# Performance work log

Hardware: AMD Instinct MI355X
Metric: run time of the kernel (lower is better)

The kernel has to match this reference:

```python
import jax, jax.numpy as jnp
import numpy as np

N, D, H, E, K = 16384, 1024, 4096, 8, 2
EPS = 1e-5


def setup_inputs() -> dict:
    key = jax.random.key(0)
    ks = jax.random.split(key, 12)
    s = 0.02
    return {
        "x": jax.random.normal(ks[0], (N, D), dtype=jnp.float32),
        "ln_g": jnp.ones((D,), jnp.float32),
        "ln_b": jnp.zeros((D,), jnp.float32),
        "r_w1": jax.random.normal(ks[1], (D, H // 2), jnp.float32) * s,
        "r_b1": jnp.zeros((H // 2,), jnp.float32),
        "r_w2": jax.random.normal(ks[2], (H // 2, E), jnp.float32) * s,
        "r_b2": jnp.zeros((E,), jnp.float32),
        "e_w1": jax.random.normal(ks[3], (E, D, H), jnp.float32) * s,
        "e_b1": jnp.zeros((E, H), jnp.float32),
        "e_w2": jax.random.normal(ks[4], (E, H, D), jnp.float32) * s,
        "e_b2": jnp.zeros((E, D), jnp.float32),
    }


def reference(x, ln_g, ln_b, r_w1, r_b1, r_w2, r_b2, e_w1, e_b1, e_w2, e_b2):
    # LayerNorm
    mu = jnp.mean(x, axis=-1, keepdims=True)
    var = jnp.mean(jnp.square(x - mu), axis=-1, keepdims=True)
    xn = (x - mu) * jax.lax.rsqrt(var + EPS) * ln_g + ln_b  # [N, D]

    # Router: Linear -> ReLU -> Linear -> softmax -> top-k, renormalize
    logits = jax.nn.relu(xn @ r_w1 + r_b1) @ r_w2 + r_b2  # [N, E]
    probs = jax.nn.softmax(logits, axis=-1)
    vals, idx = jax.lax.top_k(probs, K)  # [N, K]
    vals = vals / jnp.sum(vals, axis=-1, keepdims=True)

    # Dense expert dispatch: loop over fixed small E, weight by combine gate
    out = jnp.zeros_like(x)
    for e in range(E):
        gate = jnp.sum(vals * (idx == e).astype(vals.dtype), axis=-1)  # [N]
        h = jax.nn.relu(xn @ e_w1[e] + e_b1[e])  # dropout in eval mode -> identity
        y = h @ e_w2[e] + e_b2[e]  # [N, D]
        out = out + gate[:, None] * y
    return x + out
```

## Files before the change

### kernel.cpp

```cpp
#include <hip/hip_runtime.h>
#include <cstdint>
#include <cstddef>

typedef unsigned short u16;
typedef __attribute__((ext_vector_type(8))) short bf16x8;
typedef __attribute__((ext_vector_type(4))) float f32x4;

#define N_TOK 16384
#define DIM   1024
#define HID   4096
#define NEXP  8
#define HR    2048
#define TAU   0.02f
#define MAXMT 264

__device__ __forceinline__ u16 f2bf(float f) {
  union { float f; uint32_t u; } x; x.f = f;
  uint32_t r = x.u + 0x7FFFu + ((x.u >> 16) & 1u);
  return (u16)(r >> 16);
}
__device__ __forceinline__ float bf2f(u16 u) {
  union { uint32_t u; float f; } x; x.u = ((uint32_t)u) << 16; return x.f;
}

__device__ __forceinline__ void async16(const void* g, const void* l) {
  auto gp = reinterpret_cast<const __attribute__((address_space(1))) uint32_t*>(
      reinterpret_cast<uintptr_t>(g));
  auto lp = reinterpret_cast<__attribute__((address_space(3))) uint32_t*>(
      reinterpret_cast<uintptr_t>(l));
  __builtin_amdgcn_global_load_lds(gp, lp, 16, 0, 0);
}

__device__ __forceinline__ unsigned xcd_swz(unsigned flat, unsigned nwg) {
  const unsigned xcd = flat & 7u, lid = flat >> 3;
  const unsigned q = nwg >> 3, r = nwg & 7u;
  return (xcd < r ? xcd * (q + 1u) : r * (q + 1u) + (xcd - r) * q) + lid;
}

template<bool SPLIT>
__global__ __launch_bounds__(256)
void transpose_cvt(const float* __restrict__ src, u16* __restrict__ hi,
                   u16* __restrict__ lo, int R, int C)
{
  __shared__ float tile[32][33];
  const size_t bofs = (size_t)blockIdx.z * R * C;
  src += bofs; hi += bofs; if (SPLIT) lo += bofs;
  const int tx = threadIdx.x, ty = threadIdx.y;
  const int c0 = blockIdx.x * 32, r0 = blockIdx.y * 32;
#pragma unroll
  for (int i = 0; i < 4; ++i)
    tile[ty + i * 8][tx] = src[(size_t)(r0 + ty + i * 8) * C + c0 + tx];
  __syncthreads();
#pragma unroll
  for (int i = 0; i < 4; ++i) {
    float v = tile[tx][ty + i * 8];
    size_t o = (size_t)(c0 + ty + i * 8) * R + r0 + tx;
    u16 h = f2bf(v);
    hi[o] = h;
    if (SPLIT) lo[o] = f2bf(v - bf2f(h));
  }
}

__global__ __launch_bounds__(256)
void ln_kernel(const float* __restrict__ x, const float* __restrict__ g,
               const float* __restrict__ b, u16* __restrict__ xh,
               u16* __restrict__ xl, float* __restrict__ out)
{
  const int row = blockIdx.x;
  const int t = threadIdx.x;
  const float4 xv = ((const float4*)(x + (size_t)row * DIM))[t];
  float s = xv.x + xv.y + xv.z + xv.w;
  float q = xv.x * xv.x + xv.y * xv.y + xv.z * xv.z + xv.w * xv.w;
#pragma unroll
  for (int off = 32; off; off >>= 1) {
    s += __shfl_down(s, off, 64);
    q += __shfl_down(q, off, 64);
  }
  __shared__ float sm[8];
  __shared__ float mu_s, rs_s;
  const int lane = t & 63, wv = t >> 6;
  if (lane == 0) { sm[wv] = s; sm[wv + 4] = q; }
  __syncthreads();
  if (t == 0) {
    float S = sm[0] + sm[1] + sm[2] + sm[3];
    float Q = sm[4] + sm[5] + sm[6] + sm[7];
    float mu = S * (1.f / DIM);
    float var = Q * (1.f / DIM) - mu * mu;
    mu_s = mu; rs_s = rsqrtf(var + 1e-5f);
  }
  __syncthreads();
  const float mu = mu_s, rs = rs_s;
  const float4 gv = ((const float4*)g)[t];
  const float4 bv = ((const float4*)b)[t];
  float n0 = (xv.x - mu) * rs * gv.x + bv.x;
  float n1 = (xv.y - mu) * rs * gv.y + bv.y;
  float n2 = (xv.z - mu) * rs * gv.z + bv.z;
  float n3 = (xv.w - mu) * rs * gv.w + bv.w;
  ushort4 h, l;
  h.x = f2bf(n0); l.x = f2bf(n0 - bf2f(h.x));
  h.y = f2bf(n1); l.y = f2bf(n1 - bf2f(h.y));
  h.z = f2bf(n2); l.z = f2bf(n2 - bf2f(h.z));
  h.w = f2bf(n3); l.w = f2bf(n3 - bf2f(h.w));
  ((ushort4*)(xh + (size_t)row * DIM))[t] = h;
  ((ushort4*)(xl + (size_t)row * DIM))[t] = l;
  ((float4*)(out + (size_t)row * DIM))[t] = xv;
}

__global__ __launch_bounds__(256)
void logits_kernel(const u16* __restrict__ HrB, const float* __restrict__ w2,
                   float* __restrict__ logits)
{
  const int row = blockIdx.x, t = threadIdx.x;
  const u16* h = HrB + (size_t)row * HR;
  const ushort4* hv = (const ushort4*)(h + t * 8);
  ushort4 h0 = hv[0], h1 = hv[1];
  u16 hh[8] = {h0.x, h0.y, h0.z, h0.w, h1.x, h1.y, h1.z, h1.w};
  float p[8] = {0, 0, 0, 0, 0, 0, 0, 0};
#pragma unroll
  for (int j = 0; j < 8; ++j) {
    const int col = t * 8 + j;
    const float v = bf2f(hh[j]);
    const float4* wp = (const float4*)(w2 + (size_t)col * 8);
    float4 a = wp[0], b = wp[1];
    p[0] += v * a.x; p[1] += v * a.y; p[2] += v * a.z; p[3] += v * a.w;
    p[4] += v * b.x; p[5] += v * b.y; p[6] += v * b.z; p[7] += v * b.w;
  }
#pragma unroll
  for (int off = 32; off; off >>= 1)
#pragma unroll
    for (int e = 0; e < 8; ++e) p[e] += __shfl_down(p[e], off, 64);
  __shared__ float sm[4][8];
  const int lane = t & 63, wv = t >> 6;
  if (lane == 0) {
#pragma unroll
    for (int e = 0; e < 8; ++e) sm[wv][e] = p[e];
  }
  __syncthreads();
  if (t < 8)
    logits[(size_t)row * 8 + t] = sm[0][t] + sm[1][t] + sm[2][t] + sm[3][t];
}

__device__ __forceinline__ void load_logits(const float* logits, const float* b2,
                                            int row, float l[8]) {
  const float4* lp = (const float4*)(logits + (size_t)row * 8);
  float4 a = lp[0], b = lp[1];
  l[0] = a.x + b2[0]; l[1] = a.y + b2[1]; l[2] = a.z + b2[2]; l[3] = a.w + b2[3];
  l[4] = b.x + b2[4]; l[5] = b.y + b2[5]; l[6] = b.z + b2[6]; l[7] = b.w + b2[7];
}
__device__ __forceinline__ void top2(const float l[8], int& i0, float& l0,
                                     int& i1, float& l1) {
  i0 = 0; l0 = l[0];
#pragma unroll
  for (int e = 1; e < 8; ++e) if (l[e] > l0) { l0 = l[e]; i0 = e; }
  i1 = -1; l1 = -1e30f;
#pragma unroll
  for (int e = 0; e < 8; ++e) if (e != i0 && l[e] > l1) { l1 = l[e]; i1 = e; }
}

__global__ __launch_bounds__(256)
void pass_flag(float* __restrict__ logits, const float* __restrict__ b2,
               int* __restrict__ fixL, int* __restrict__ cntFix)
{
  __shared__ int lcnt;
  __shared__ int base;
  const int t = threadIdx.x;
  const int row = blockIdx.x * 256 + t;
  if (t == 0) lcnt = 0;
  float l[8]; load_logits(logits, b2, row, l);
  int i0, i1; float l0, l1;
  top2(l, i0, l0, i1, l1);
  float l2 = -1e30f;
#pragma unroll
  for (int e = 0; e < 8; ++e)
    if (e != i0 && e != i1 && l[e] > l2) l2 = l[e];
  const bool flag = (l1 - l2) < TAU;
  __syncthreads();
  int r = 0;
  if (flag) r = atomicAdd(&lcnt, 1);
  __syncthreads();
  if (t == 0) base = atomicAdd(cntFix, lcnt);
  __syncthreads();
  if (flag) {
    fixL[base + r] = row;
    float4 z = {0.f, 0.f, 0.f, 0.f};
    ((float4*)(logits + (size_t)row * 8))[0] = z;
    ((float4*)(logits + (size_t)row * 8))[1] = z;
  }
}

__global__ __launch_bounds__(256)
void pass_count(const float* __restrict__ logits, const float* __restrict__ b2,
                int* __restrict__ cnts)
{
  __shared__ int lcnt[NEXP];
  const int t = threadIdx.x;
  const int row = blockIdx.x * 256 + t;
  if (t < NEXP) lcnt[t] = 0;
  float l[8]; load_logits(logits, b2, row, l);
  int i0, i1; float l0, l1;
  top2(l, i0, l0, i1, l1);
  __syncthreads();
  atomicAdd(&lcnt[i0], 1);
  atomicAdd(&lcnt[i1], 1);
  __syncthreads();
  if (t < NEXP) atomicAdd(&cnts[t], lcnt[t]);
}

__global__ void scan_kernel(const int* __restrict__ cnts, int* __restrict__ offs,
                            int* __restrict__ tileOffs)
{
  if (threadIdx.x == 0) {
    int s = 0, ts = 0;
#pragma unroll
    for (int e = 0; e < NEXP; ++e) {
      offs[e] = s; s += cnts[e];
      tileOffs[e] = ts; ts += (cnts[e] + 127) >> 7;
    }
    offs[NEXP] = s;
    tileOffs[NEXP] = ts;
  }
}

__global__ __launch_bounds__(256)
void pass_scatter(const float* __restrict__ logits, const float* __restrict__ b2,
                  const int* __restrict__ offs, int* __restrict__ cnts2,
                  int* __restrict__ rowsC, float* __restrict__ gateC)
{
  __shared__ int lcnt[NEXP];
  __shared__ int sbase[NEXP];
  const int t = threadIdx.x;
  const int row = blockIdx.x * 256 + t;
  if (t < NEXP) lcnt[t] = 0;
  float l[8]; load_logits(logits, b2, row, l);
  int i0, i1; float l0, l1;
  top2(l, i0, l0, i1, l1);
  float tt = expf(l1 - l0);
  float g0 = 1.f / (1.f + tt);
  float g1 = tt / (1.f + tt);
  __syncthreads();
  int r0 = atomicAdd(&lcnt[i0], 1);
  int r1 = atomicAdd(&lcnt[i1], 1);
  __syncthreads();
  if (t < NEXP) sbase[t] = atomicAdd(&cnts2[t], lcnt[t]);
  __syncthreads();
  int p0 = offs[i0] + sbase[i0] + r0;
  int p1 = offs[i1] + sbase[i1] + r1;
  rowsC[p0] = row; gateC[p0] = g0;
  rowsC[p1] = row; gateC[p1] = g1;
}

template<int EPI, bool GATHER>
__global__ __launch_bounds__(512, 4)
void gemm_moe(const u16* __restrict__ A0, const u16* __restrict__ B0,
              int lda, int ldb, int K, int NT,
              size_t bStrideE, int biasStrideE,
              const int* __restrict__ counts,
              const int* __restrict__ offs, const int* __restrict__ tileOffs,
              const int* __restrict__ rowsC, const float* __restrict__ gatesC,
              const float* __restrict__ bias,
              u16* __restrict__ Cbf, float* __restrict__ Cf32, int ldc)
{
  const unsigned swz = xcd_swz(blockIdx.x, gridDim.x);
  const int mt = (int)(swz / (unsigned)NT);
  if (mt >= tileOffs[NEXP]) return;
  int e = 0;
#pragma unroll
  for (int i = 1; i < NEXP; ++i) if (tileOffs[i] <= mt) e = i;
  const int m0 = (mt - tileOffs[e]) * 128;
  const int n0 = (int)(swz % (unsigned)NT) * 256;
  const int Mq = counts[e];
  if (m0 >= Mq) return;

  const int off = offs[e];
  const int* rows = rowsC + off;
  const u16* B = B0 + (size_t)e * bStrideE;
  const float* bi = bias + (size_t)e * biasStrideE;

  __shared__ alignas(16) u16 As[4][128 * 32];
  __shared__ alignas(16) u16 Bs[3][256 * 32];

  const int t = threadIdx.x;
  const int numK = K >> 5;

  const int rloc = t >> 2;
  const int cb = ((t & 3) << 4) ^ (((t >> 5) & 1) << 5);
  const int csrc = cb >> 1;
  const int arow0 = m0 + rloc;
  const int amc = arow0 < Mq ? arow0 : (Mq - 1);
  const size_t agr = GATHER ? (size_t)rows[amc] : (size_t)(off + amc);
  const u16* aSrc = A0 + agr * lda + csrc;
  const u16* bSrc0 = B + (size_t)(n0 + rloc) * ldb + csrc;
  const u16* bSrc1 = B + (size_t)(n0 + 128 + rloc) * ldb + csrc;

  const int lane = t & 63, wv = t >> 6;
  const int wm = wv >> 2;
  const int wn = wv & 3;
  const int fr = lane & 15, fq = lane >> 4;

  int aIdx[4], bIdx[4];
#pragma unroll
  for (int mf = 0; mf < 4; ++mf) {
    const int r = wm * 64 + mf * 16 + fr;
    aIdx[mf] = r * 32 + ((fq * 8) ^ (((r >> 3) & 1) << 4));
  }
#pragma unroll
  for (int nf = 0; nf < 4; ++nf) {
    const int rb = wn * 64 + nf * 16 + fr;
    bIdx[nf] = rb * 32 + ((fq * 8) ^ (((rb >> 3) & 1) << 4));
  }

  f32x4 acc[4][4];
#pragma unroll
  for (int i = 0; i < 4; ++i)
#pragma unroll
    for (int j = 0; j < 4; ++j) acc[i][j] = (f32x4){0.f, 0.f, 0.f, 0.f};

#pragma unroll
  for (int h = 0; h < 3; ++h)
    async16(aSrc + h * 32, &As[h][t * 8]);
#pragma unroll
  for (int h = 0; h < 2; ++h) {
    async16(bSrc0 + h * 32, &Bs[h][t * 8]);
    async16(bSrc1 + h * 32, &Bs[h][4096 + t * 8]);
  }
  asm volatile("s_waitcnt vmcnt(2)" ::: "memory");
  __builtin_amdgcn_s_barrier();
  __builtin_amdgcn_sched_barrier(0);

  int bR = 0;
  int bW = 2;
  for (int T = 0; T < numK; ++T) {
    if (T + 2 < numK) {
      async16(bSrc0 + (T + 2) * 32, &Bs[bW][t * 8]);
      async16(bSrc1 + (T + 2) * 32, &Bs[bW][4096 + t * 8]);
    }
    if (T + 3 < numK) async16(aSrc + (T + 3) * 32, &As[(T + 3) & 3][t * 8]);

    const u16* aLds = As[T & 3];
    const u16* bLds = Bs[bR];
    bf16x8 aF[4], bF[4];
#pragma unroll
    for (int i = 0; i < 4; ++i) {
      aF[i] = *(const bf16x8*)&aLds[aIdx[i]];
      bF[i] = *(const bf16x8*)&bLds[bIdx[i]];
    }
    __builtin_amdgcn_s_setprio(1);
#pragma unroll
    for (int mf = 0; mf < 4; ++mf)
#pragma unroll
      for (int nf = 0; nf < 4; ++nf)
        acc[mf][nf] = __builtin_amdgcn_mfma_f32_16x16x32_bf16(
            aF[mf], bF[nf], acc[mf][nf], 0, 0, 0);
    __builtin_amdgcn_s_setprio(0);
    __builtin_amdgcn_sched_barrier(0);

    const int rem = numK - T;
    if (rem >= 4) {
      if (T == 0) { asm volatile("s_waitcnt vmcnt(3)" ::: "memory"); }
      else        { asm volatile("s_waitcnt vmcnt(4)" ::: "memory"); }
    }
    else if (rem == 3) { asm volatile("s_waitcnt vmcnt(3)" ::: "memory"); }
    else               { asm volatile("s_waitcnt vmcnt(0)" ::: "memory"); }
    __builtin_amdgcn_s_barrier();
    __builtin_amdgcn_sched_barrier(0);

    bR = (bR == 2) ? 0 : bR + 1;
    bW = (bW == 2) ? 0 : bW + 1;
  }

  float bv[4];
#pragma unroll
  for (int nf = 0; nf < 4; ++nf) bv[nf] = bi[n0 + wn * 64 + nf * 16 + fr];

#pragma unroll
  for (int mf = 0; mf < 4; ++mf)
#pragma unroll
    for (int r = 0; r < 4; ++r) {
      const int m = m0 + wm * 64 + mf * 16 + fq * 4 + r;
      if (m < Mq) {
        if constexpr (EPI == 2) {
          const size_t orow = (size_t)rows[m];
          const float g = gatesC[off + m];
#pragma unroll
          for (int nf = 0; nf < 4; ++nf) {
            const int n = n0 + wn * 64 + nf * 16 + fr;
            atomicAdd(&Cf32[orow * ldc + n], g * (acc[mf][nf][r] + bv[nf]));
          }
        } else {
#pragma unroll
          for (int nf = 0; nf < 4; ++nf) {
            const int n = n0 + wn * 64 + nf * 16 + fr;
            Cbf[(size_t)(off + m) * ldc + n] =
                f2bf(fmaxf(acc[mf][nf][r] + bv[nf], 0.f));
          }
        }
      }
    }
}

template<bool SPLIT, int EPI, bool GATHER>
__global__ __launch_bounds__(256, 2)
void gemm_bt(const u16* __restrict__ A0, const u16* __restrict__ A1,
             const u16* __restrict__ B0, const u16* __restrict__ B1,
             int lda, int ldb, int K, int M,
             const int* __restrict__ counts, int expertArg,
             const int* __restrict__ offs,
             const int* __restrict__ rowsC, const float* __restrict__ gatesC,
             const float* __restrict__ bias,
             const float* __restrict__ w2, float* __restrict__ logits,
             u16* __restrict__ Cbf, float* __restrict__ Cf32, int ldc)
{
  int expert, m0, n0;
  if (counts == nullptr) {
    const unsigned nwg = gridDim.x * gridDim.y;
    const unsigned flat = blockIdx.y * gridDim.x + blockIdx.x;
    const unsigned swz = xcd_swz(flat, nwg);
    expert = expertArg;
    m0 = (int)(swz / gridDim.x) * 128;
    n0 = (int)(swz % gridDim.x) * 128;
  } else {
    expert = expertArg;
    m0 = blockIdx.y * 128;
    n0 = blockIdx.x * 128;
  }

  const int Mq = counts ? counts[expert] : M;
  if (m0 >= Mq) return;
  const int off = offs ? offs[expert] : 0;
  const int* rows = rowsC ? rowsC + off : nullptr;
  const float* gates = gatesC ? gatesC + off : nullptr;
  const u16* B = B0;
  const u16* Bl = SPLIT ? B1 : nullptr;
  const float* bi = bias;
  const int z = (int)blockIdx.z;
  const int zOff = z * K;

  __shared__ u16 As0[128 * 32], Bs0[128 * 32];
  __shared__ u16 As1[SPLIT ? 128 * 32 : 8], Bs1[SPLIT ? 128 * 32 : 8];

  const int t = threadIdx.x;
  size_t aoff[2]; int acodd[2]; size_t boff[2];
#pragma unroll
  for (int i = 0; i < 2; ++i) {
    int gdx = i * 256 + t;
    int ar = gdx >> 2, ac = (gdx & 3) * 8;
    int am = m0 + ar;
    int amc = am < Mq ? am : (Mq - 1);
    int agr = GATHER ? rows[amc] : amc;
    aoff[i] = (size_t)agr * lda + ac + zOff;
    boff[i] = (size_t)(n0 + ar) * ldb + ac + zOff;
    acodd[i] = gdx * 8;
  }

  f32x4 acc[4][4];
#pragma unroll
  for (int i = 0; i < 4; ++i)
#pragma unroll
    for (int j = 0; j < 4; ++j) acc[i][j] = (f32x4){0.f, 0.f, 0.f, 0.f};

  const int lane = t & 63, wv = t >> 6;
  const int wm = (wv >> 1) * 64, wn = (wv & 1) * 64;
  const int fr = lane & 15, fq = lane >> 4;

  for (int k0 = 0; k0 < K; k0 += 32) {
    __syncthreads();
#pragma unroll
    for (int i = 0; i < 2; ++i) {
      async16(A0 + aoff[i] + k0, &As0[acodd[i]]);
      async16(B + boff[i] + k0, &Bs0[acodd[i]]);
      if (SPLIT) {
        async16(A1 + aoff[i] + k0, &As1[acodd[i]]);
        async16(Bl + boff[i] + k0, &Bs1[acodd[i]]);
      }
    }
    __syncthreads();
    bf16x8 af[4], bfr[4], af1[4], bf1[4];
#pragma unroll
    for (int xi = 0; xi < 4; ++xi) {
      af[xi]  = *(const bf16x8*)&As0[(wm + xi * 16 + fr) * 32 + fq * 8];
      bfr[xi] = *(const bf16x8*)&Bs0[(wn + xi * 16 + fr) * 32 + fq * 8];
      if (SPLIT) {
        af1[xi] = *(const bf16x8*)&As1[(wm + xi * 16 + fr) * 32 + fq * 8];
        bf1[xi] = *(const bf16x8*)&Bs1[(wn + xi * 16 + fr) * 32 + fq * 8];
      }
    }
#pragma unroll
    for (int mt = 0; mt < 4; ++mt)
#pragma unroll
      for (int nt = 0; nt < 4; ++nt) {
        acc[mt][nt] = __builtin_amdgcn_mfma_f32_16x16x32_bf16(af[mt], bfr[nt], acc[mt][nt], 0, 0, 0);
        if (SPLIT) {
          acc[mt][nt] = __builtin_amdgcn_mfma_f32_16x16x32_bf16(af[mt], bf1[nt], acc[mt][nt], 0, 0, 0);
          acc[mt][nt] = __builtin_amdgcn_mfma_f32_16x16x32_bf16(af1[mt], bfr[nt], acc[mt][nt], 0, 0, 0);
        }
      }
  }

  if constexpr (EPI == 3) {
    float w2v[4][8]; float b1v[4];
#pragma unroll
    for (int nt = 0; nt < 4; ++nt) {
      const int n = n0 + wn + nt * 16 + fr;
      b1v[nt] = bi[n];
      const float4* wp = (const float4*)(w2 + (size_t)n * 8);
      float4 wa = wp[0], wb = wp[1];
      w2v[nt][0] = wa.x; w2v[nt][1] = wa.y; w2v[nt][2] = wa.z; w2v[nt][3] = wa.w;
      w2v[nt][4] = wb.x; w2v[nt][5] = wb.y; w2v[nt][6] = wb.z; w2v[nt][7] = wb.w;
    }
#pragma unroll
    for (int mt = 0; mt < 4; ++mt) {
      float pe[4][8];
#pragma unroll
      for (int r = 0; r < 4; ++r)
#pragma unroll
        for (int ee = 0; ee < 8; ++ee) pe[r][ee] = 0.f;
#pragma unroll
      for (int nt = 0; nt < 4; ++nt)
#pragma unroll
        for (int r = 0; r < 4; ++r) {
          float v = fmaxf(acc[mt][nt][r] + b1v[nt], 0.f);
#pragma unroll
          for (int ee = 0; ee < 8; ++ee) pe[r][ee] += v * w2v[nt][ee];
        }
#pragma unroll
      for (int offx = 1; offx < 16; offx <<= 1)
#pragma unroll
        for (int r = 0; r < 4; ++r)
#pragma unroll
          for (int ee = 0; ee < 8; ++ee)
            pe[r][ee] += __shfl_xor(pe[r][ee], offx, 64);
      if (fr == 0) {
#pragma unroll
        for (int r = 0; r < 4; ++r) {
          const int m = m0 + wm + mt * 16 + fq * 4 + r;
          if (m < Mq) {
            const int lrow = GATHER ? rows[m] : m;
#pragma unroll
            for (int ee = 0; ee < 8; ++ee)
              atomicAdd(&logits[(size_t)lrow * 8 + ee], pe[r][ee]);
          }
        }
      }
    }
    return;
  }

#pragma unroll
  for (int mt = 0; mt < 4; ++mt) {
#pragma unroll
    for (int nt = 0; nt < 4; ++nt) {
      const int n = n0 + wn + nt * 16 + fr;
      const float bvv = (z == 0) ? bi[n] : 0.f;
#pragma unroll
      for (int r = 0; r < 4; ++r) {
        const int m = m0 + wm + mt * 16 + fq * 4 + r;
        if (m < Mq) {
          float v = acc[mt][nt][r] + bvv;
          if constexpr (EPI == 1) {
            Cbf[(size_t)m * ldc + n] = f2bf(fmaxf(v, 0.f));
          } else {
            atomicAdd(&Cf32[(size_t)rows[m] * ldc + n], gates[m] * v);
          }
        }
      }
    }
  }
}

extern "C" void kernel_launch(void* const* d_in, const int* in_sizes, int n_in,
                              void* d_out, int out_size, void* d_ws, size_t ws_size,
                              hipStream_t stream)
{
  const float* x    = (const float*)d_in[0];
  const float* ln_g = (const float*)d_in[1];
  const float* ln_b = (const float*)d_in[2];
  const float* r_w1 = (const float*)d_in[3];
  const float* r_b1 = (const float*)d_in[4];
  const float* r_w2 = (const float*)d_in[5];
  const float* r_b2 = (const float*)d_in[6];
  const float* e_w1 = (const float*)d_in[7];
  const float* e_b1 = (const float*)d_in[8];
  const float* e_w2 = (const float*)d_in[9];
  const float* e_b2 = (const float*)d_in[10];
  float* out = (float*)d_out;

  char* ws = (char*)d_ws;
  const size_t MB = 1024ull * 1024ull;
  u16*   xnhi = (u16*)(ws);
  u16*   xnlo = (u16*)(ws + 32 * MB);
  u16*   rw1h = (u16*)(ws + 64 * MB);
  u16*   rw1l = (u16*)(ws + 68 * MB);
  u16*   ew1t = (u16*)(ws + 72 * MB);
  u16*   ew2t = (u16*)(ws + 136 * MB);
  float* logits = (float*)(ws + 200 * MB);
  int*   rowsC  = (int*)(ws + 200 * MB + 512 * 1024);
  float* gateC  = (float*)(ws + 200 * MB + 640 * 1024);
  int*   fixL   = (int*)(ws + 200 * MB + 768 * 1024);
  int*   cntb   = (int*)(ws + 200 * MB + 832 * 1024);
  int*   cnts   = cntb;
  int*   cnts2  = cntb + 8;
  int*   offs   = cntb + 16;
  int*   cntFix = cntb + 25;
  int*   tileOffs = cntb + 32;
  u16*   Hbuf = (u16*)(ws + 201 * MB);
  u16*   HrB  = Hbuf;
  (void)in_sizes; (void)n_in; (void)out_size;

  const bool fused = ws_size >= 458ull * MB;

  hipMemsetAsync(cntb, 0, 256, stream);

  dim3 tb(32, 8);
  transpose_cvt<true ><<<dim3(HR / 32, DIM / 32, 1), tb, 0, stream>>>(r_w1, rw1h, rw1l, DIM, HR);
  transpose_cvt<false><<<dim3(HID / 32, DIM / 32, NEXP), tb, 0, stream>>>(e_w1, ew1t, nullptr, DIM, HID);
  transpose_cvt<false><<<dim3(DIM / 32, HID / 32, NEXP), tb, 0, stream>>>(e_w2, ew2t, nullptr, HID, DIM);

  ln_kernel<<<N_TOK, 256, 0, stream>>>(x, ln_g, ln_b, xnhi, xnlo, out);

  gemm_bt<false, 1, false><<<dim3(HR / 128, N_TOK / 128), 256, 0, stream>>>(
      xnhi, nullptr, rw1h, nullptr, DIM, DIM, DIM, N_TOK,
      nullptr, 0, nullptr, nullptr, nullptr, r_b1, nullptr, nullptr,
      HrB, nullptr, HR);

  logits_kernel<<<N_TOK, 256, 0, stream>>>(HrB, r_w2, logits);

  pass_flag<<<N_TOK / 256, 256, 0, stream>>>(logits, r_b2, fixL, cntFix);

  gemm_bt<true, 3, true><<<dim3(HR / 128, N_TOK / 128), 256, 0, stream>>>(
      xnhi, xnlo, rw1h, rw1l, DIM, DIM, DIM, N_TOK,
      cntFix, 0, nullptr, fixL, nullptr, r_b1, r_w2, logits,
      nullptr, nullptr, 0);

  pass_count<<<N_TOK / 256, 256, 0, stream>>>(logits, r_b2, cnts);
  scan_kernel<<<1, 64, 0, stream>>>(cnts, offs, tileOffs);
  pass_scatter<<<N_TOK / 256, 256, 0, stream>>>(logits, r_b2, offs, cnts2, rowsC, gateC);

  if (fused) {
    gemm_moe<1, true><<<dim3((HID / 256) * MAXMT), 512, 0, stream>>>(
        xnhi, ew1t, DIM, DIM, DIM, HID / 256,
        (size_t)HID * DIM, HID,
        cnts, offs, tileOffs, rowsC, nullptr, e_b1,
        Hbuf, nullptr, HID);
    gemm_moe<2, false><<<dim3((DIM / 256) * MAXMT), 512, 0, stream>>>(
        Hbuf, ew2t, HID, HID, HID, DIM / 256,
        (size_t)DIM * HID, DIM,
        cnts, offs, tileOffs, rowsC, gateC, e_b2,
        nullptr, out, DIM);
  } else {
    for (int e = 0; e < NEXP; ++e) {
      gemm_bt<false, 1, true><<<dim3(HID / 128, N_TOK / 128), 256, 0, stream>>>(
          xnhi, nullptr, ew1t + (size_t)e * HID * DIM, nullptr,
          DIM, DIM, DIM, N_TOK,
          cnts, e, offs, rowsC, nullptr, e_b1 + (size_t)e * HID, nullptr, nullptr,
          Hbuf, nullptr, HID);
      gemm_bt<false, 2, false><<<dim3(DIM / 128, N_TOK / 128, 2), 256, 0, stream>>>(
          Hbuf, nullptr, ew2t + (size_t)e * DIM * HID, nullptr,
          HID, HID, HID / 2, N_TOK,
          cnts, e, offs, rowsC, gateC, e_b2 + (size_t)e * DIM, nullptr, nullptr,
          nullptr, out, DIM);
    }
  }
}
```

Baseline: 1.371 ms.

## Halve MoE GEMM block to 4 waves with 128x64 per-wave tiles

The expert GEMM now runs with 256 threads (4 waves) instead of 512 (8 waves) per 128x256 tile. Each wave owns a 128x64 slice, so it holds 8x4 accumulator fragments and issues more MFMAs per LDS fragment load, raising register reuse. Each thread also issues twice as many async global-to-LDS copies, and the vmcnt waits are rescaled to match. The trade is fewer waves to hide latency and higher register pressure under launch_bounds(256,2).

```diff
diff --git a/kernel.cpp b/kernel.cpp
--- a/kernel.cpp
+++ b/kernel.cpp
@@ -250,7 +250,7 @@
 }
 
 template<int EPI, bool GATHER>
-__global__ __launch_bounds__(512, 4)
+__global__ __launch_bounds__(256, 2)
 void gemm_moe(const u16* __restrict__ A0, const u16* __restrict__ B0,
               int lda, int ldb, int K, int NT,
               size_t bStrideE, int biasStrideE,
@@ -282,25 +282,36 @@
   const int t = threadIdx.x;
   const int numK = K >> 5;
 
-  const int rloc = t >> 2;
-  const int cb = ((t & 3) << 4) ^ (((t >> 5) & 1) << 5);
-  const int csrc = cb >> 1;
-  const int arow0 = m0 + rloc;
-  const int amc = arow0 < Mq ? arow0 : (Mq - 1);
-  const size_t agr = GATHER ? (size_t)rows[amc] : (size_t)(off + amc);
-  const u16* aSrc = A0 + agr * lda + csrc;
-  const u16* bSrc0 = B + (size_t)(n0 + rloc) * ldb + csrc;
-  const u16* bSrc1 = B + (size_t)(n0 + 128 + rloc) * ldb + csrc;
+  const u16* aptr[2]; int adst[2];
+#pragma unroll
+  for (int i = 0; i < 2; ++i) {
+    const int gdx = i * 256 + t;
+    const int ar = gdx >> 2;
+    const int cb = ((gdx & 3) << 4) ^ (((gdx >> 5) & 1) << 5);
+    const int am = m0 + ar;
+    const int amc = am < Mq ? am : (Mq - 1);
+    const size_t agr = GATHER ? (size_t)rows[amc] : (size_t)(off + amc);
+    aptr[i] = A0 + agr * lda + (cb >> 1);
+    adst[i] = gdx * 8;
+  }
+  const u16* bptr[4]; int bdst[4];
+#pragma unroll
+  for (int i = 0; i < 4; ++i) {
+    const int gdx = i * 256 + t;
+    const int br = gdx >> 2;
+    const int cb = ((gdx & 3) << 4) ^ (((gdx >> 5) & 1) << 5);
+    bptr[i] = B + (size_t)(n0 + br) * ldb + (cb >> 1);
+    bdst[i] = gdx * 8;
+  }
 
   const int lane = t & 63, wv = t >> 6;
-  const int wm = wv >> 2;
-  const int wn = wv & 3;
+  const int wn = wv;
   const int fr = lane & 15, fq = lane >> 4;
 
-  int aIdx[4], bIdx[4];
-#pragma unroll
-  for (int mf = 0; mf < 4; ++mf) {
-    const int r = wm * 64 + mf * 16 + fr;
+  int aIdx[8], bIdx[4];
+#pragma unroll
+  for (int mf = 0; mf < 8; ++mf) {
+    const int r = mf * 16 + fr;
     aIdx[mf] = r * 32 + ((fq * 8) ^ (((r >> 3) & 1) << 4));
   }
 #pragma unroll
@@ -309,21 +320,23 @@
     bIdx[nf] = rb * 32 + ((fq * 8) ^ (((rb >> 3) & 1) << 4));
   }
 
-  f32x4 acc[4][4];
-#pragma unroll
-  for (int i = 0; i < 4; ++i)
+  f32x4 acc[8][4];
+#pragma unroll
+  for (int i = 0; i < 8; ++i)
 #pragma unroll
     for (int j = 0; j < 4; ++j) acc[i][j] = (f32x4){0.f, 0.f, 0.f, 0.f};
 
 #pragma unroll
-  for (int h = 0; h < 3; ++h)
-    async16(aSrc + h * 32, &As[h][t * 8]);
-#pragma unroll
-  for (int h = 0; h < 2; ++h) {
-    async16(bSrc0 + h * 32, &Bs[h][t * 8]);
-    async16(bSrc1 + h * 32, &Bs[h][4096 + t * 8]);
-  }
-  asm volatile("s_waitcnt vmcnt(2)" ::: "memory");
+  for (int h = 0; h < 3; ++h) {
+    async16(aptr[0] + h * 32, &As[h][adst[0]]);
+    async16(aptr[1] + h * 32, &As[h][adst[1]]);
+  }
+#pragma unroll
+  for (int h = 0; h < 2; ++h)
+#pragma unroll
+    for (int i = 0; i < 4; ++i)
+      async16(bptr[i] + h * 32, &Bs[h][bdst[i]]);
+  asm volatile("s_waitcnt vmcnt(4)" ::: "memory");
   __builtin_amdgcn_s_barrier();
   __builtin_amdgcn_sched_barrier(0);
 
@@ -331,22 +344,26 @@
   int bW = 2;
   for (int T = 0; T < numK; ++T) {
     if (T + 2 < numK) {
-      async16(bSrc0 + (T + 2) * 32, &Bs[bW][t * 8]);
-      async16(bSrc1 + (T + 2) * 32, &Bs[bW][4096 + t * 8]);
-    }
-    if (T + 3 < numK) async16(aSrc + (T + 3) * 32, &As[(T + 3) & 3][t * 8]);
-
-    const u16* aLds = As[T & 3];
-    const u16* bLds = Bs[bR];
-    bf16x8 aF[4], bF[4];
-#pragma unroll
-    for (int i = 0; i < 4; ++i) {
-      aF[i] = *(const bf16x8*)&aLds[aIdx[i]];
-      bF[i] = *(const bf16x8*)&bLds[bIdx[i]];
-    }
+#pragma unroll
+      for (int i = 0; i < 4; ++i)
+        async16(bptr[i] + (size_t)(T + 2) * 32, &Bs[bW][bdst[i]]);
+    }
+    if (T + 3 < numK) {
+      async16(aptr[0] + (size_t)(T + 3) * 32, &As[(T + 3) & 3][adst[0]]);
+      async16(aptr[1] + (size_t)(T + 3) * 32, &As[(T + 3) & 3][adst[1]]);
+    }
+
+    const u16* aL = As[T & 3];
+    const u16* bL = Bs[bR];
+    bf16x8 aF[8], bF[4];
+#pragma unroll
+    for (int mf = 0; mf < 8; ++mf) aF[mf] = *(const bf16x8*)&aL[aIdx[mf]];
+#pragma unroll
+    for (int nf = 0; nf < 4; ++nf) bF[nf] = *(const bf16x8*)&bL[bIdx[nf]];
+
     __builtin_amdgcn_s_setprio(1);
 #pragma unroll
-    for (int mf = 0; mf < 4; ++mf)
+    for (int mf = 0; mf < 8; ++mf)
 #pragma unroll
       for (int nf = 0; nf < 4; ++nf)
         acc[mf][nf] = __builtin_amdgcn_mfma_f32_16x16x32_bf16(
@@ -355,11 +372,9 @@
     __builtin_amdgcn_sched_barrier(0);
 
     const int rem = numK - T;
-    if (rem >= 4) {
-      if (T == 0) { asm volatile("s_waitcnt vmcnt(3)" ::: "memory"); }
-      else        { asm volatile("s_waitcnt vmcnt(4)" ::: "memory"); }
-    }
-    else if (rem == 3) { asm volatile("s_waitcnt vmcnt(3)" ::: "memory"); }
+    if (T == 0)        { asm volatile("s_waitcnt vmcnt(6)" ::: "memory"); }
+    else if (rem >= 4) { asm volatile("s_waitcnt vmcnt(8)" ::: "memory"); }
+    else if (rem == 3) { asm volatile("s_waitcnt vmcnt(6)" ::: "memory"); }
     else               { asm volatile("s_waitcnt vmcnt(0)" ::: "memory"); }
     __builtin_amdgcn_s_barrier();
     __builtin_amdgcn_sched_barrier(0);
@@ -373,10 +388,10 @@
   for (int nf = 0; nf < 4; ++nf) bv[nf] = bi[n0 + wn * 64 + nf * 16 + fr];
 
 #pragma unroll
-  for (int mf = 0; mf < 4; ++mf)
+  for (int mf = 0; mf < 8; ++mf)
 #pragma unroll
     for (int r = 0; r < 4; ++r) {
-      const int m = m0 + wm * 64 + mf * 16 + fq * 4 + r;
+      const int m = m0 + mf * 16 + fq * 4 + r;
       if (m < Mq) {
         if constexpr (EPI == 2) {
           const size_t orow = (size_t)rows[m];
@@ -636,12 +651,12 @@
   pass_scatter<<<N_TOK / 256, 256, 0, stream>>>(logits, r_b2, offs, cnts2, rowsC, gateC);
 
   if (fused) {
-    gemm_moe<1, true><<<dim3((HID / 256) * MAXMT), 512, 0, stream>>>(
+    gemm_moe<1, true><<<dim3((HID / 256) * MAXMT), 256, 0, stream>>>(
         xnhi, ew1t, DIM, DIM, DIM, HID / 256,
         (size_t)HID * DIM, HID,
         cnts, offs, tileOffs, rowsC, nullptr, e_b1,
         Hbuf, nullptr, HID);
-    gemm_moe<2, false><<<dim3((DIM / 256) * MAXMT), 512, 0, stream>>>(
+    gemm_moe<2, false><<<dim3((DIM / 256) * MAXMT), 256, 0, stream>>>(
         Hbuf, ew2t, HID, HID, HID, DIM / 256,
         (size_t)DIM * HID, DIM,
         cnts, offs, tileOffs, rowsC, gateC, e_b2,
```

After: 1.373 ms. Within noise of the previous version (+0.1%).

## Shrink MoE GEMM tiles to 128x128 with 256 threads and reuse for router GEMM

Applied to the files above, without the earlier changes.

Changes the grouped MoE GEMM from 128x256 tiles with 512 threads to 128x128 tiles with 256 threads. A and B now share a uniform 3-stage LDS pipeline, and the wait counts are rewritten to match. A DENSE template variant is added and replaces the older gemm_bt kernel for the router's first linear layer. Smaller tiles launch more blocks and use less LDS per block, which may raise occupancy. In exchange, each block reuses operands less and more global traffic goes to B.

```diff
diff --git a/kernel.cpp b/kernel.cpp
--- a/kernel.cpp
+++ b/kernel.cpp
@@ -249,10 +249,10 @@
   rowsC[p1] = row; gateC[p1] = g1;
 }
 
-template<int EPI, bool GATHER>
-__global__ __launch_bounds__(512, 4)
+template<int EPI, bool GATHER, bool DENSE>
+__global__ __launch_bounds__(256, 3)
 void gemm_moe(const u16* __restrict__ A0, const u16* __restrict__ B0,
-              int lda, int ldb, int K, int NT,
+              int lda, int ldb, int K, int NT, int Mdense,
               size_t bStrideE, int biasStrideE,
               const int* __restrict__ counts,
               const int* __restrict__ offs, const int* __restrict__ tileOffs,
@@ -262,39 +262,49 @@
 {
   const unsigned swz = xcd_swz(blockIdx.x, gridDim.x);
   const int mt = (int)(swz / (unsigned)NT);
-  if (mt >= tileOffs[NEXP]) return;
-  int e = 0;
-#pragma unroll
-  for (int i = 1; i < NEXP; ++i) if (tileOffs[i] <= mt) e = i;
-  const int m0 = (mt - tileOffs[e]) * 128;
-  const int n0 = (int)(swz % (unsigned)NT) * 256;
-  const int Mq = counts[e];
-  if (m0 >= Mq) return;
-
-  const int off = offs[e];
-  const int* rows = rowsC + off;
+  int e, m0, Mq, off;
+  if constexpr (DENSE) {
+    if (mt >= Mdense / 128) return;
+    e = 0; m0 = mt * 128; Mq = Mdense; off = 0;
+  } else {
+    if (mt >= tileOffs[NEXP]) return;
+    e = 0;
+#pragma unroll
+    for (int i = 1; i < NEXP; ++i) if (tileOffs[i] <= mt) e = i;
+    m0 = (mt - tileOffs[e]) * 128;
+    Mq = counts[e];
+    if (m0 >= Mq) return;
+    off = offs[e];
+  }
+  const int n0 = (int)(swz % (unsigned)NT) * 128;
+  const int* rows = DENSE ? nullptr : (rowsC + off);
   const u16* B = B0 + (size_t)e * bStrideE;
   const float* bi = bias + (size_t)e * biasStrideE;
 
-  __shared__ alignas(16) u16 As[4][128 * 32];
-  __shared__ alignas(16) u16 Bs[3][256 * 32];
+  __shared__ alignas(16) u16 As[3][128 * 32];
+  __shared__ alignas(16) u16 Bs[3][128 * 32];
 
   const int t = threadIdx.x;
   const int numK = K >> 5;
 
-  const int rloc = t >> 2;
-  const int cb = ((t & 3) << 4) ^ (((t >> 5) & 1) << 5);
-  const int csrc = cb >> 1;
-  const int arow0 = m0 + rloc;
-  const int amc = arow0 < Mq ? arow0 : (Mq - 1);
-  const size_t agr = GATHER ? (size_t)rows[amc] : (size_t)(off + amc);
-  const u16* aSrc = A0 + agr * lda + csrc;
-  const u16* bSrc0 = B + (size_t)(n0 + rloc) * ldb + csrc;
-  const u16* bSrc1 = B + (size_t)(n0 + 128 + rloc) * ldb + csrc;
+  const u16* aptr[2]; const u16* bptr[2]; int sdst[2];
+#pragma unroll
+  for (int i = 0; i < 2; ++i) {
+    const int gdx = i * 256 + t;
+    const int r = gdx >> 2;
+    const int cb = ((gdx & 3) << 4) ^ (((gdx >> 5) & 1) << 5);
+    const int cs = cb >> 1;
+    int amc = (m0 + r) < Mq ? (m0 + r) : (Mq - 1);
+    const size_t agr = DENSE ? (size_t)(m0 + r)
+                             : (GATHER ? (size_t)rows[amc] : (size_t)(off + amc));
+    aptr[i] = A0 + agr * lda + cs;
+    bptr[i] = B + (size_t)(n0 + r) * ldb + cs;
+    sdst[i] = gdx * 8;
+  }
 
   const int lane = t & 63, wv = t >> 6;
-  const int wm = wv >> 2;
-  const int wn = wv & 3;
+  const int wm = wv >> 1;
+  const int wn = wv & 1;
   const int fr = lane & 15, fq = lane >> 4;
 
   int aIdx[4], bIdx[4];
@@ -316,33 +326,33 @@
     for (int j = 0; j < 4; ++j) acc[i][j] = (f32x4){0.f, 0.f, 0.f, 0.f};
 
 #pragma unroll
-  for (int h = 0; h < 3; ++h)
-    async16(aSrc + h * 32, &As[h][t * 8]);
-#pragma unroll
   for (int h = 0; h < 2; ++h) {
-    async16(bSrc0 + h * 32, &Bs[h][t * 8]);
-    async16(bSrc1 + h * 32, &Bs[h][4096 + t * 8]);
-  }
-  asm volatile("s_waitcnt vmcnt(2)" ::: "memory");
+    async16(bptr[0] + h * 32, &Bs[h][sdst[0]]);
+    async16(bptr[1] + h * 32, &Bs[h][sdst[1]]);
+    async16(aptr[0] + h * 32, &As[h][sdst[0]]);
+    async16(aptr[1] + h * 32, &As[h][sdst[1]]);
+  }
+  asm volatile("s_waitcnt vmcnt(4)" ::: "memory");
   __builtin_amdgcn_s_barrier();
   __builtin_amdgcn_sched_barrier(0);
 
-  int bR = 0;
-  int bW = 2;
+  int sR = 0;
+  int sW = 2;
   for (int T = 0; T < numK; ++T) {
     if (T + 2 < numK) {
-      async16(bSrc0 + (T + 2) * 32, &Bs[bW][t * 8]);
-      async16(bSrc1 + (T + 2) * 32, &Bs[bW][4096 + t * 8]);
-    }
-    if (T + 3 < numK) async16(aSrc + (T + 3) * 32, &As[(T + 3) & 3][t * 8]);
-
-    const u16* aLds = As[T & 3];
-    const u16* bLds = Bs[bR];
+      async16(bptr[0] + (size_t)(T + 2) * 32, &Bs[sW][sdst[0]]);
+      async16(bptr[1] + (size_t)(T + 2) * 32, &Bs[sW][sdst[1]]);
+      async16(aptr[0] + (size_t)(T + 2) * 32, &As[sW][sdst[0]]);
+      async16(aptr[1] + (size_t)(T + 2) * 32, &As[sW][sdst[1]]);
+    }
+
+    const u16* aL = As[sR];
+    const u16* bL = Bs[sR];
     bf16x8 aF[4], bF[4];
 #pragma unroll
     for (int i = 0; i < 4; ++i) {
-      aF[i] = *(const bf16x8*)&aLds[aIdx[i]];
-      bF[i] = *(const bf16x8*)&bLds[bIdx[i]];
+      aF[i] = *(const bf16x8*)&aL[aIdx[i]];
+      bF[i] = *(const bf16x8*)&bL[bIdx[i]];
     }
     __builtin_amdgcn_s_setprio(1);
 #pragma unroll
@@ -355,17 +365,18 @@
     __builtin_amdgcn_sched_barrier(0);
 
     const int rem = numK - T;
-    if (rem >= 4) {
-      if (T == 0) { asm volatile("s_waitcnt vmcnt(3)" ::: "memory"); }
-      else        { asm volatile("s_waitcnt vmcnt(4)" ::: "memory"); }
-    }
-    else if (rem == 3) { asm volatile("s_waitcnt vmcnt(3)" ::: "memory"); }
-    else               { asm volatile("s_waitcnt vmcnt(0)" ::: "memory"); }
-    __builtin_amdgcn_s_barrier();
-    __builtin_amdgcn_sched_barrier(0);
-
-    bR = (bR == 2) ? 0 : bR + 1;
-    bW = (bW == 2) ? 0 : bW + 1;
+    if (rem >= 3) {
+      asm volatile("s_waitcnt vmcnt(4)" ::: "memory");
+      __builtin_amdgcn_s_barrier();
+      __builtin_amdgcn_sched_barrier(0);
+    } else if (rem == 2) {
+      asm volatile("s_waitcnt vmcnt(0)" ::: "memory");
+      __builtin_amdgcn_s_barrier();
+      __builtin_amdgcn_sched_barrier(0);
+    }
+
+    sR = (sR == 2) ? 0 : sR + 1;
+    sW = (sW == 2) ? 0 : sW + 1;
   }
 
   float bv[4];
@@ -617,9 +628,9 @@
 
   ln_kernel<<<N_TOK, 256, 0, stream>>>(x, ln_g, ln_b, xnhi, xnlo, out);
 
-  gemm_bt<false, 1, false><<<dim3(HR / 128, N_TOK / 128), 256, 0, stream>>>(
-      xnhi, nullptr, rw1h, nullptr, DIM, DIM, DIM, N_TOK,
-      nullptr, 0, nullptr, nullptr, nullptr, r_b1, nullptr, nullptr,
+  gemm_moe<1, false, true><<<dim3((HR / 128) * (N_TOK / 128)), 256, 0, stream>>>(
+      xnhi, rw1h, DIM, DIM, DIM, HR / 128, N_TOK, 0, 0,
+      nullptr, nullptr, nullptr, nullptr, nullptr, r_b1,
       HrB, nullptr, HR);
 
   logits_kernel<<<N_TOK, 256, 0, stream>>>(HrB, r_w2, logits);
@@ -636,13 +647,13 @@
   pass_scatter<<<N_TOK / 256, 256, 0, stream>>>(logits, r_b2, offs, cnts2, rowsC, gateC);
 
   if (fused) {
-    gemm_moe<1, true><<<dim3((HID / 256) * MAXMT), 512, 0, stream>>>(
-        xnhi, ew1t, DIM, DIM, DIM, HID / 256,
+    gemm_moe<1, true, false><<<dim3((HID / 128) * MAXMT), 256, 0, stream>>>(
+        xnhi, ew1t, DIM, DIM, DIM, HID / 128, 0,
         (size_t)HID * DIM, HID,
         cnts, offs, tileOffs, rowsC, nullptr, e_b1,
         Hbuf, nullptr, HID);
-    gemm_moe<2, false><<<dim3((DIM / 256) * MAXMT), 512, 0, stream>>>(
-        Hbuf, ew2t, HID, HID, HID, DIM / 256,
+    gemm_moe<2, false, false><<<dim3((DIM / 128) * MAXMT), 256, 0, stream>>>(
+        Hbuf, ew2t, HID, HID, HID, DIM / 128, 0,
         (size_t)DIM * HID, DIM,
         cnts, offs, tileOffs, rowsC, gateC, e_b2,
         nullptr, out, DIM);
```

Result: slower. 1.445 ms (+5.3%).
